# Optimization experiments

Hardware: AMD Instinct MI355X
Metric: run time of the kernel (lower is better)

Reference implementation:

```python
import jax, jax.numpy as jnp
import numpy as np


def setup_inputs() -> dict:
    key = jax.random.key(0)
    ks = jax.random.split(key, 6)
    B, S, DK = 4, 2048, 1024
    scale = 1.0 / np.sqrt(DK)  # keep weight magnitudes sane like torch init
    return {
        "q": jax.random.normal(ks[0], (B, S, DK), jnp.float32),
        "k": jax.random.normal(ks[1], (B, S, DK), jnp.float32),
        "v": jax.random.normal(ks[2], (B, S, DK), jnp.float32),
        "wq": jax.random.normal(ks[3], (DK, DK), jnp.float32) * scale,
        "wk": jax.random.normal(ks[4], (DK, DK), jnp.float32) * scale,
        "wv": jax.random.normal(ks[5], (DK, DK), jnp.float32) * scale,
    }


def reference(q, k, v, wq, wk, wv):
    dk = q.shape[-1]
    # nn.Linear: y = x @ W^T  (weights stored [out, in])
    qp = jnp.einsum("bsd,ed->bse", q, wq)
    kp = jnp.einsum("bsd,ed->bse", k, wk)
    vp = jnp.einsum("bsd,ed->bse", v, wv)
    norm = 1.0 / jnp.sqrt(jnp.asarray(dk, qp.dtype))
    s = jnp.einsum("bqd,bkd->bqk", qp, kp) * norm  # [B, S, S]
    # module computes exp(s)/sum(exp(s)) manually; mathematically softmax
    e = jnp.exp(s)
    attention = e / jnp.sum(e, axis=-1, keepdims=True)
    # dropout is identity in eval mode (deterministic reference)
    return jnp.einsum("bqk,bkd->bqd", attention, vp)
```

## Files before the change

kernel.cpp:

```cpp
#include <hip/hip_runtime.h>

typedef _Float16 f16;
typedef _Float16 f16x4 __attribute__((ext_vector_type(4)));
typedef _Float16 f16x8 __attribute__((ext_vector_type(8)));
typedef float    fx4   __attribute__((ext_vector_type(4)));

#define MODE_PROJ   0
#define MODE_SCORES 1
#define MODE_PV     2

constexpr int Bsz = 4;
constexpr int S   = 2048;
constexpr int DK  = 1024;
constexpr int BM = 128, BN = 128, BK = 64;
constexpr long SD   = (long)S * DK;
constexpr long SS   = (long)S * S;
constexpr long BIGN = (long)Bsz * S * DK;

__device__ __forceinline__ void glds16(const f16* g, f16* l) {
    __builtin_amdgcn_global_load_lds(
        (const __attribute__((address_space(1))) void*)g,
        (__attribute__((address_space(3))) void*)l, 16, 0, 0);
}

__global__ __launch_bounds__(256)
void convert_kernel(const float* q, const float* k, const float* v,
                    const float* wq, const float* wk, const float* wv)
{
    int bx = blockIdx.x;
    const float* src;
    int blk;
    if (bx < 12288) {
        int t = bx >> 12; blk = bx & 4095;
        src = (t == 0) ? q : (t == 1) ? k : v;
    } else {
        int u = bx - 12288;
        int t = u >> 9; blk = u & 511;
        src = (t == 0) ? wq : (t == 1) ? wk : wv;
    }
    size_t off = (size_t)blk * 2048 + (size_t)threadIdx.x * 8;
    float4 f0 = *(const float4*)(src + off);
    float4 f1 = *(const float4*)(src + off + 4);
    __syncthreads();
    f16x8 h = {(f16)f0.x, (f16)f0.y, (f16)f0.z, (f16)f0.w,
               (f16)f1.x, (f16)f1.y, (f16)f1.z, (f16)f1.w};
    *(f16x8*)((char*)src + (size_t)blk * 8192 + (size_t)threadIdx.x * 16) = h;
}

__device__ __forceinline__ size_t pp(int r, int c) {
    return ((size_t)(r >> 1) << 12) + ((r & 1) << 10) + c;
}

template<int MODE>
__global__ __launch_bounds__(256, 4)
void gemm_kernel(const f16* A0, const f16* A1, const f16* A2,
                 const f16* B0, const f16* B1, const f16* B2,
                 void* O0, void* O1, float* rowsum,
                 int lda, int ldb, int K, int ldo)
{
    __shared__ f16 lA[BM * BK];
    __shared__ f16 lB[BN * BK];

    const int tid = threadIdx.x;
    const int id  = blockIdx.x;
    const int z   = blockIdx.y;
    int row0, col0;
    if constexpr (MODE == MODE_PROJ) { row0 = (id & 63) * BM; col0 = (id >> 6) * BN; }
    else                             { row0 = (id & 15) * BM; col0 = (id >> 4) * BN; }

    const int lane = tid & 63;
    const int quad = lane >> 4;
    const int cn   = lane & 15;
    const int w    = tid >> 6;
    const int wm   = w >> 1;
    const int wn   = w & 1;

    const f16 *Ap, *Bp;
    if constexpr (MODE == MODE_PROJ) {
        Ap = (z == 0) ? A0 : (z == 1) ? A1 : A2;
        Bp = (z == 0) ? B0 : (z == 1) ? B1 : B2;
    } else if constexpr (MODE == MODE_SCORES) {
        Ap = A0 + (long)z * SD;  Bp = B0 + (long)z * SD;
        rowsum += (long)z * S;
    } else {
        Ap = A0 + (long)z * SS;  Bp = B0 + (long)z * SD;
        rowsum += (long)z * S;
    }

    fx4 acc[4][4];
    #pragma unroll
    for (int mt = 0; mt < 4; ++mt)
        #pragma unroll
        for (int nt = 0; nt < 4; ++nt)
            acc[mt][nt] = (fx4){0.f, 0.f, 0.f, 0.f};

    const int lr8 = lane >> 3;
    const int swc = (lane & 7) ^ lr8;
    const int lcS = swc << 3;

    for (int k0 = 0; k0 < K; k0 += BK) {
        __syncthreads();
        #pragma unroll
        for (int i = 0; i < 4; ++i) {
            int rb = w * 32 + i * 8;
            if constexpr (MODE == MODE_PROJ) {
                glds16(Ap + pp(row0 + rb + lr8, k0 + lcS), &lA[rb * BK]);
                glds16(Bp + pp(col0 + rb + lr8, k0 + lcS), &lB[rb * BK]);
            } else {
                glds16(Ap + (size_t)(row0 + rb + lr8) * lda + k0 + lcS, &lA[rb * BK]);
                glds16(Bp + (size_t)(col0 + rb + lr8) * ldb + k0 + lcS, &lB[rb * BK]);
            }
        }
        __syncthreads();

        #pragma unroll
        for (int kh = 0; kh < 2; ++kh) {
            f16x8 af[4], bf[4];
            #pragma unroll
            for (int mt = 0; mt < 4; ++mt) {
                int r = wm * 64 + mt * 16 + cn;
                int ch = ((kh << 2) | quad) ^ (r & 7);
                af[mt] = *(const f16x8*)&lA[r * BK + ch * 8];
            }
            #pragma unroll
            for (int nt = 0; nt < 4; ++nt) {
                int r = wn * 64 + nt * 16 + cn;
                int ch = ((kh << 2) | quad) ^ (r & 7);
                bf[nt] = *(const f16x8*)&lB[r * BK + ch * 8];
            }
            #pragma unroll
            for (int mt = 0; mt < 4; ++mt)
                #pragma unroll
                for (int nt = 0; nt < 4; ++nt)
                    acc[mt][nt] = __builtin_amdgcn_mfma_f32_16x16x32_f16(
                        af[mt], bf[nt], acc[mt][nt], 0, 0, 0);
        }
    }

    if constexpr (MODE == MODE_PROJ) {
        if (z < 2) {
            f16* O = (f16*)O0 + (long)z * BIGN;
            #pragma unroll
            for (int mt = 0; mt < 4; ++mt) {
                int r0 = row0 + wm * 64 + mt * 16 + quad * 4;
                #pragma unroll
                for (int nt = 0; nt < 4; ++nt) {
                    int c = col0 + wn * 64 + nt * 16 + cn;
                    #pragma unroll
                    for (int reg = 0; reg < 4; ++reg)
                        O[(size_t)(r0 + reg) * DK + c] = (f16)acc[mt][nt][reg];
                }
            }
        } else {
            #pragma unroll
            for (int mt = 0; mt < 4; ++mt) {
                int r0 = row0 + wm * 64 + mt * 16 + quad * 4;
                int b  = r0 >> 11;
                int s  = r0 & 2047;
                f16* O = (f16*)O1 + (long)b * SD;
                #pragma unroll
                for (int nt = 0; nt < 4; ++nt) {
                    int c = col0 + wn * 64 + nt * 16 + cn;
                    f16x4 h = {(f16)acc[mt][nt][0], (f16)acc[mt][nt][1],
                               (f16)acc[mt][nt][2], (f16)acc[mt][nt][3]};
                    *(f16x4*)&O[(size_t)c * S + s] = h;
                }
            }
        }
    } else if constexpr (MODE == MODE_SCORES) {
        f16* O = (f16*)O0 + (long)z * SS;
        const float sl2e = 0.03125f * 1.44269504f;
        float rs[4][4];
        #pragma unroll
        for (int mt = 0; mt < 4; ++mt)
            #pragma unroll
            for (int reg = 0; reg < 4; ++reg) rs[mt][reg] = 0.f;
        #pragma unroll
        for (int mt = 0; mt < 4; ++mt) {
            int r0 = row0 + wm * 64 + mt * 16 + quad * 4;
            #pragma unroll
            for (int nt = 0; nt < 4; ++nt) {
                int c = col0 + wn * 64 + nt * 16 + cn;
                #pragma unroll
                for (int reg = 0; reg < 4; ++reg) {
                    float vv = exp2f(acc[mt][nt][reg] * sl2e);
                    rs[mt][reg] += vv;
                    O[(size_t)(r0 + reg) * ldo + c] = (f16)vv;
                }
            }
        }
        #pragma unroll
        for (int mt = 0; mt < 4; ++mt) {
            int r0 = row0 + wm * 64 + mt * 16 + quad * 4;
            #pragma unroll
            for (int reg = 0; reg < 4; ++reg) {
                float vv = rs[mt][reg];
                vv += __shfl_xor(vv, 1);
                vv += __shfl_xor(vv, 2);
                vv += __shfl_xor(vv, 4);
                vv += __shfl_xor(vv, 8);
                if (cn == 0) atomicAdd(&rowsum[r0 + reg], vv);
            }
        }
    } else {
        float* O = (float*)O0 + (long)z * SD;
        #pragma unroll
        for (int mt = 0; mt < 4; ++mt) {
            int r0 = row0 + wm * 64 + mt * 16 + quad * 4;
            fx4 rsv = *(const fx4*)&rowsum[r0];
            fx4 inv = {1.f / rsv[0], 1.f / rsv[1], 1.f / rsv[2], 1.f / rsv[3]};
            #pragma unroll
            for (int nt = 0; nt < 4; ++nt) {
                int c = col0 + wn * 64 + nt * 16 + cn;
                #pragma unroll
                for (int reg = 0; reg < 4; ++reg)
                    O[(size_t)(r0 + reg) * ldo + c] = acc[mt][nt][reg] * inv[reg];
            }
        }
    }
}

extern "C" void kernel_launch(void* const* d_in, const int* in_sizes, int n_in,
                              void* d_out, int out_size, void* d_ws, size_t ws_size,
                              hipStream_t stream) {
    const float* q  = (const float*)d_in[0];
    const float* k  = (const float*)d_in[1];
    const float* v  = (const float*)d_in[2];
    const float* wq = (const float*)d_in[3];
    const float* wk = (const float*)d_in[4];
    const float* wv = (const float*)d_in[5];
    float* out = (float*)d_out;

    char* ws = (char*)d_ws;
    f16*   qp     = (f16*)(ws);
    f16*   kp     = (f16*)(ws + ((size_t)16 << 20));
    f16*   vpT    = (f16*)(ws + ((size_t)32 << 20));
    f16*   E      = (f16*)(ws + ((size_t)48 << 20));
    float* rowsum = (float*)(ws + ((size_t)80 << 20));

    hipMemsetAsync(rowsum, 0, (size_t)Bsz * S * sizeof(float), stream);

    convert_kernel<<<13824, 256, 0, stream>>>(q, k, v, wq, wk, wv);

    const f16* qh  = (const f16*)q;
    const f16* kh  = (const f16*)k;
    const f16* vh  = (const f16*)v;
    const f16* wqh = (const f16*)wq;
    const f16* wkh = (const f16*)wk;
    const f16* wvh = (const f16*)wv;

    dim3 blk(256);
    gemm_kernel<MODE_PROJ><<<dim3(512, 3), blk, 0, stream>>>(
        qh, kh, vh, wqh, wkh, wvh, qp, vpT, nullptr, DK, DK, DK, DK);
    gemm_kernel<MODE_SCORES><<<dim3(256, 4), blk, 0, stream>>>(
        qp, nullptr, nullptr, kp, nullptr, nullptr, E, nullptr, rowsum,
        DK, DK, DK, S);
    gemm_kernel<MODE_PV><<<dim3(128, 4), blk, 0, stream>>>(
        E, nullptr, nullptr, vpT, nullptr, nullptr, out, nullptr, rowsum,
        S, S, S, DK);
}
```

Measured before the change: 296.2 us.

## Double-buffer LDS and widen GEMM tile to 128x256 with 8 waves

```diff
diff --git a/kernel.cpp b/kernel.cpp
--- a/kernel.cpp
+++ b/kernel.cpp
@@ -12,7 +12,7 @@
 constexpr int Bsz = 4;
 constexpr int S   = 2048;
 constexpr int DK  = 1024;
-constexpr int BM = 128, BN = 128, BK = 64;
+constexpr int BM = 128, BN = 256, BK = 64;
 constexpr long SD   = (long)S * DK;
 constexpr long SS   = (long)S * S;
 constexpr long BIGN = (long)Bsz * S * DK;
@@ -52,14 +52,14 @@
 }
 
 template<int MODE>
-__global__ __launch_bounds__(256, 4)
+__global__ __launch_bounds__(512, 2)
 void gemm_kernel(const f16* A0, const f16* A1, const f16* A2,
                  const f16* B0, const f16* B1, const f16* B2,
                  void* O0, void* O1, float* rowsum,
                  int lda, int ldb, int K, int ldo)
 {
-    __shared__ f16 lA[BM * BK];
-    __shared__ f16 lB[BN * BK];
+    __shared__ __attribute__((aligned(16))) f16 lA[2][BM * BK];
+    __shared__ __attribute__((aligned(16))) f16 lB[2][BN * BK];
 
     const int tid = threadIdx.x;
     const int id  = blockIdx.x;
@@ -72,8 +72,8 @@
     const int quad = lane >> 4;
     const int cn   = lane & 15;
     const int w    = tid >> 6;
-    const int wm   = w >> 1;
-    const int wn   = w & 1;
+    const int wm   = w >> 2;
+    const int wn   = w & 3;
 
     const f16 *Ap, *Bp;
     if constexpr (MODE == MODE_PROJ) {
@@ -98,44 +98,98 @@
     const int swc = (lane & 7) ^ lr8;
     const int lcS = swc << 3;
 
-    for (int k0 = 0; k0 < K; k0 += BK) {
+    f16x8 af[4];
+    f16x8 bf[8];
+
+#define STAGE(BUF, K0) do {                                                          \
+    _Pragma("unroll")                                                                \
+    for (int i_ = 0; i_ < 2; ++i_) {                                                 \
+        int rb_ = w * 16 + i_ * 8;                                                   \
+        if constexpr (MODE == MODE_PROJ)                                             \
+            glds16(Ap + pp(row0 + rb_ + lr8, (K0) + lcS), &lA[BUF][rb_ * BK]);       \
+        else                                                                         \
+            glds16(Ap + (size_t)(row0 + rb_ + lr8) * lda + (K0) + lcS,               \
+                   &lA[BUF][rb_ * BK]);                                              \
+    }                                                                                \
+    _Pragma("unroll")                                                                \
+    for (int i_ = 0; i_ < 4; ++i_) {                                                 \
+        int rb_ = w * 32 + i_ * 8;                                                   \
+        if constexpr (MODE == MODE_PROJ)                                             \
+            glds16(Bp + pp(col0 + rb_ + lr8, (K0) + lcS), &lB[BUF][rb_ * BK]);       \
+        else                                                                         \
+            glds16(Bp + (size_t)(col0 + rb_ + lr8) * ldb + (K0) + lcS,               \
+                   &lB[BUF][rb_ * BK]);                                              \
+    }                                                                                \
+} while (0)
+
+#define LDA_FRAGS(BUF, MH) do {                                                      \
+    _Pragma("unroll")                                                                \
+    for (int m_ = 0; m_ < 2; ++m_)                                                   \
+        _Pragma("unroll")                                                            \
+        for (int kk_ = 0; kk_ < 2; ++kk_) {                                          \
+            int r_  = wm * 64 + ((MH) * 2 + m_) * 16 + cn;                           \
+            int ch_ = ((kk_ << 2) | quad) ^ (r_ & 7);                                \
+            af[m_ * 2 + kk_] = *(const f16x8*)&lA[BUF][r_ * BK + ch_ * 8];           \
+        }                                                                            \
+} while (0)
+
+#define LDB_FRAGS(BUF, NH) do {                                                      \
+    _Pragma("unroll")                                                                \
+    for (int n_ = 0; n_ < 2; ++n_)                                                   \
+        _Pragma("unroll")                                                            \
+        for (int kk_ = 0; kk_ < 2; ++kk_) {                                          \
+            int nt_ = (NH) * 2 + n_;                                                 \
+            int r_  = wn * 64 + nt_ * 16 + cn;                                       \
+            int ch_ = ((kk_ << 2) | quad) ^ (r_ & 7);                                \
+            bf[nt_ * 2 + kk_] = *(const f16x8*)&lB[BUF][r_ * BK + ch_ * 8];          \
+        }                                                                            \
+} while (0)
+
+#define QUAD_MFMA(MH, NH) do {                                                       \
+    __builtin_amdgcn_s_setprio(1);                                                   \
+    _Pragma("unroll")                                                                \
+    for (int m_ = 0; m_ < 2; ++m_)                                                   \
+        _Pragma("unroll")                                                            \
+        for (int n_ = 0; n_ < 2; ++n_) {                                             \
+            _Pragma("unroll")                                                        \
+            for (int kk_ = 0; kk_ < 2; ++kk_)                                        \
+                acc[(MH) * 2 + m_][(NH) * 2 + n_] =                                  \
+                    __builtin_amdgcn_mfma_f32_16x16x32_f16(                          \
+                        af[m_ * 2 + kk_], bf[((NH) * 2 + n_) * 2 + kk_],             \
+                        acc[(MH) * 2 + m_][(NH) * 2 + n_], 0, 0, 0);                 \
+        }                                                                            \
+    __builtin_amdgcn_s_setprio(0);                                                   \
+} while (0)
+
+    const int ntile = K / BK;
+    STAGE(0, 0);
+    __syncthreads();
+    int bufc = 0;
+    for (int t = 0; t < ntile; ++t) {
+        const int k0 = t * BK;
+        LDA_FRAGS(bufc, 0);
+        LDB_FRAGS(bufc, 0);
+        if (t + 1 < ntile) STAGE(bufc ^ 1, k0 + BK);
+        __builtin_amdgcn_s_barrier();
+        QUAD_MFMA(0, 0);
+        __builtin_amdgcn_s_barrier();
+        LDB_FRAGS(bufc, 1);
+        __builtin_amdgcn_s_barrier();
+        QUAD_MFMA(0, 1);
+        __builtin_amdgcn_s_barrier();
+        LDA_FRAGS(bufc, 1);
+        __builtin_amdgcn_s_barrier();
+        QUAD_MFMA(1, 1);
+        __builtin_amdgcn_s_barrier();
+        QUAD_MFMA(1, 0);
         __syncthreads();
-        #pragma unroll
-        for (int i = 0; i < 4; ++i) {
-            int rb = w * 32 + i * 8;
-            if constexpr (MODE == MODE_PROJ) {
-                glds16(Ap + pp(row0 + rb + lr8, k0 + lcS), &lA[rb * BK]);
-                glds16(Bp + pp(col0 + rb + lr8, k0 + lcS), &lB[rb * BK]);
-            } else {
-                glds16(Ap + (size_t)(row0 + rb + lr8) * lda + k0 + lcS, &lA[rb * BK]);
-                glds16(Bp + (size_t)(col0 + rb + lr8) * ldb + k0 + lcS, &lB[rb * BK]);
-            }
-        }
-        __syncthreads();
-
-        #pragma unroll
-        for (int kh = 0; kh < 2; ++kh) {
-            f16x8 af[4], bf[4];
-            #pragma unroll
-            for (int mt = 0; mt < 4; ++mt) {
-                int r = wm * 64 + mt * 16 + cn;
-                int ch = ((kh << 2) | quad) ^ (r & 7);
-                af[mt] = *(const f16x8*)&lA[r * BK + ch * 8];
-            }
-            #pragma unroll
-            for (int nt = 0; nt < 4; ++nt) {
-                int r = wn * 64 + nt * 16 + cn;
-                int ch = ((kh << 2) | quad) ^ (r & 7);
-                bf[nt] = *(const f16x8*)&lB[r * BK + ch * 8];
-            }
-            #pragma unroll
-            for (int mt = 0; mt < 4; ++mt)
-                #pragma unroll
-                for (int nt = 0; nt < 4; ++nt)
-                    acc[mt][nt] = __builtin_amdgcn_mfma_f32_16x16x32_f16(
-                        af[mt], bf[nt], acc[mt][nt], 0, 0, 0);
-        }
+        bufc ^= 1;
     }
+
+#undef STAGE
+#undef LDA_FRAGS
+#undef LDB_FRAGS
+#undef QUAD_MFMA
 
     if constexpr (MODE == MODE_PROJ) {
         if (z < 2) {
@@ -249,13 +303,13 @@
     const f16* wkh = (const f16*)wk;
     const f16* wvh = (const f16*)wv;
 
-    dim3 blk(256);
-    gemm_kernel<MODE_PROJ><<<dim3(512, 3), blk, 0, stream>>>(
+    dim3 blk(512);
+    gemm_kernel<MODE_PROJ><<<dim3(256, 3), blk, 0, stream>>>(
         qh, kh, vh, wqh, wkh, wvh, qp, vpT, nullptr, DK, DK, DK, DK);
-    gemm_kernel<MODE_SCORES><<<dim3(256, 4), blk, 0, stream>>>(
+    gemm_kernel<MODE_SCORES><<<dim3(128, 4), blk, 0, stream>>>(
         qp, nullptr, nullptr, kp, nullptr, nullptr, E, nullptr, rowsum,
         DK, DK, DK, S);
-    gemm_kernel<MODE_PV><<<dim3(128, 4), blk, 0, stream>>>(
+    gemm_kernel<MODE_PV><<<dim3(64, 4), blk, 0, stream>>>(
         E, nullptr, nullptr, vpT, nullptr, nullptr, out, nullptr, rowsum,
         S, S, S, DK);
 }
```

Measured after the change: 309.0 us. 1.04x slower.

## Add 256x256-tile 8-wave pipelined GEMM for projection and score stages

Applied to the files above, without the earlier changes.

```diff
diff --git a/kernel.cpp b/kernel.cpp
--- a/kernel.cpp
+++ b/kernel.cpp
@@ -51,6 +51,265 @@
     return ((size_t)(r >> 1) << 12) + ((r & 1) << 10) + c;
 }
 
+
+#define VW6 asm volatile("s_waitcnt vmcnt(6)" ::: "memory")
+#define VW4 asm volatile("s_waitcnt vmcnt(4)" ::: "memory")
+#define VW2 asm volatile("s_waitcnt vmcnt(2)" ::: "memory")
+#define VW0 asm volatile("s_waitcnt vmcnt(0)" ::: "memory")
+#define VWX do {} while (0)
+
+template<int MODE>
+__global__ __launch_bounds__(512, 2)
+void gemm8p_kernel(const f16* A0_, const f16* A1_, const f16* A2_,
+                   const f16* B0_, const f16* B1_, const f16* B2_,
+                   void* O0, void* O1, float* rowsum,
+                   int lda, int ldb, int K, int ldo)
+{
+    __shared__ __attribute__((aligned(16))) f16 lA[2][2][128 * 64];
+    __shared__ __attribute__((aligned(16))) f16 lB[2][2][128 * 64];
+
+    const int tid = threadIdx.x;
+    const int id  = blockIdx.x;
+    const int z   = blockIdx.y;
+    int row0, col0;
+    if constexpr (MODE == MODE_PROJ) { row0 = (id & 31) * 256; col0 = (id >> 5) * 256; }
+    else                             { row0 = (id & 7)  * 256; col0 = (id >> 3) * 256; }
+
+    const int lane = tid & 63;
+    const int quad = lane >> 4;
+    const int cn   = lane & 15;
+    const int w    = tid >> 6;
+    const int wm   = w >> 2;
+    const int wn   = w & 3;
+
+    const f16 *Ap, *Bp;
+    if constexpr (MODE == MODE_PROJ) {
+        Ap = (z == 0) ? A0_ : (z == 1) ? A1_ : A2_;
+        Bp = (z == 0) ? B0_ : (z == 1) ? B1_ : B2_;
+    } else {
+        Ap = A0_ + (long)z * SD;  Bp = B0_ + (long)z * SD;
+        rowsum += (long)z * S;
+    }
+
+    fx4 acc[8][4];
+    #pragma unroll
+    for (int am = 0; am < 8; ++am)
+        #pragma unroll
+        for (int an = 0; an < 4; ++an)
+            acc[am][an] = (fx4){0.f, 0.f, 0.f, 0.f};
+
+    const int lr8 = lane >> 3;
+    const int swc = (lane & 7) ^ lr8;
+    const int lcS = swc << 3;
+
+    f16x8 af[8];
+    f16x8 bf0[4];
+    f16x8 bf1[4];
+
+#define STAGE_A0(BUF, K0) do {                                               \
+    _Pragma("unroll")                                                        \
+    for (int i_ = 0; i_ < 2; ++i_) {                                         \
+        int Lb_ = w * 16 + i_ * 8;                                           \
+        int rb_ = ((Lb_ >> 6) << 7) | (Lb_ & 63);                            \
+        f16* d_ = &lA[BUF][rb_ >> 7][(rb_ & 127) * 64];                      \
+        int gr_ = row0 + rb_ + lr8;                                          \
+        if constexpr (MODE == MODE_PROJ)                                     \
+            glds16(Ap + pp(gr_, (K0) + lcS), d_);                            \
+        else                                                                 \
+            glds16(Ap + (size_t)gr_ * lda + (K0) + lcS, d_);                 \
+    }                                                                        \
+} while (0)
+
+#define STAGE_A1(BUF, K0) do {                                               \
+    _Pragma("unroll")                                                        \
+    for (int i_ = 0; i_ < 2; ++i_) {                                         \
+        int Lb_ = w * 16 + i_ * 8;                                           \
+        int rb_ = (((Lb_ >> 6) << 7) | (Lb_ & 63)) + 64;                     \
+        f16* d_ = &lA[BUF][rb_ >> 7][(rb_ & 127) * 64];                      \
+        int gr_ = row0 + rb_ + lr8;                                          \
+        if constexpr (MODE == MODE_PROJ)                                     \
+            glds16(Ap + pp(gr_, (K0) + lcS), d_);                            \
+        else                                                                 \
+            glds16(Ap + (size_t)gr_ * lda + (K0) + lcS, d_);                 \
+    }                                                                        \
+} while (0)
+
+#define STAGE_B0(BUF, K0) do {                                               \
+    _Pragma("unroll")                                                        \
+    for (int i_ = 0; i_ < 2; ++i_) {                                         \
+        int Lb_ = w * 16 + i_ * 8;                                           \
+        int rb_ = ((Lb_ >> 5) << 6) | (Lb_ & 31);                            \
+        f16* d_ = &lB[BUF][rb_ >> 7][(rb_ & 127) * 64];                      \
+        int gr_ = col0 + rb_ + lr8;                                          \
+        if constexpr (MODE == MODE_PROJ)                                     \
+            glds16(Bp + pp(gr_, (K0) + lcS), d_);                            \
+        else                                                                 \
+            glds16(Bp + (size_t)gr_ * ldb + (K0) + lcS, d_);                 \
+    }                                                                        \
+} while (0)
+
+#define STAGE_B1(BUF, K0) do {                                               \
+    _Pragma("unroll")                                                        \
+    for (int i_ = 0; i_ < 2; ++i_) {                                         \
+        int Lb_ = w * 16 + i_ * 8;                                           \
+        int rb_ = (((Lb_ >> 5) << 6) | (Lb_ & 31)) + 32;                     \
+        f16* d_ = &lB[BUF][rb_ >> 7][(rb_ & 127) * 64];                      \
+        int gr_ = col0 + rb_ + lr8;                                          \
+        if constexpr (MODE == MODE_PROJ)                                     \
+            glds16(Bp + pp(gr_, (K0) + lcS), d_);                            \
+        else                                                                 \
+            glds16(Bp + (size_t)gr_ * ldb + (K0) + lcS, d_);                 \
+    }                                                                        \
+} while (0)
+
+#define LDA(BUF, MH) do {                                                    \
+    _Pragma("unroll")                                                        \
+    for (int mf_ = 0; mf_ < 4; ++mf_)                                        \
+        _Pragma("unroll")                                                    \
+        for (int kk_ = 0; kk_ < 2; ++kk_) {                                  \
+            int rr_ = (MH) * 64 + mf_ * 16 + cn;                             \
+            int ch_ = ((kk_ << 2) | quad) ^ (cn & 7);                        \
+            af[mf_ * 2 + kk_] = *(const f16x8*)&lA[BUF][wm][rr_ * 64 + ch_ * 8]; \
+        }                                                                    \
+} while (0)
+
+#define LDB(BUF, NH, BFA) do {                                               \
+    _Pragma("unroll")                                                        \
+    for (int nf_ = 0; nf_ < 2; ++nf_)                                        \
+        _Pragma("unroll")                                                    \
+        for (int kk_ = 0; kk_ < 2; ++kk_) {                                  \
+            int rr_ = (wn & 1) * 64 + (NH) * 32 + nf_ * 16 + cn;             \
+            int ch_ = ((kk_ << 2) | quad) ^ (cn & 7);                        \
+            BFA[nf_ * 2 + kk_] = *(const f16x8*)&lB[BUF][wn >> 1][rr_ * 64 + ch_ * 8]; \
+        }                                                                    \
+} while (0)
+
+#define PH_MFMA(MH, NH, BFA) do {                                            \
+    __builtin_amdgcn_s_setprio(1);                                           \
+    _Pragma("unroll")                                                        \
+    for (int mf_ = 0; mf_ < 4; ++mf_)                                        \
+        _Pragma("unroll")                                                    \
+        for (int nf_ = 0; nf_ < 2; ++nf_)                                    \
+            _Pragma("unroll")                                                \
+            for (int kk_ = 0; kk_ < 2; ++kk_)                                \
+                acc[(MH) * 4 + mf_][(NH) * 2 + nf_] =                        \
+                    __builtin_amdgcn_mfma_f32_16x16x32_f16(                  \
+                        af[mf_ * 2 + kk_], BFA[nf_ * 2 + kk_],               \
+                        acc[(MH) * 4 + mf_][(NH) * 2 + nf_], 0, 0, 0);       \
+    __builtin_amdgcn_s_setprio(0);                                           \
+} while (0)
+
+#define TILE(K0, BUF, STG, A0N, W0S, W1S, W2S, W3S) do {                     \
+                                                    \
+    LDA(BUF, 0);                                                             \
+    LDB(BUF, 0, bf0);                                                        \
+    if (STG) STAGE_B0((BUF) ^ 1, (K0) + BK);                                 \
+    __builtin_amdgcn_s_barrier();                                            \
+    PH_MFMA(0, 0, bf0);                                                      \
+    W0S; __builtin_amdgcn_s_barrier();                                       \
+                                                    \
+    LDB(BUF, 1, bf1);                                                        \
+    if (STG) STAGE_B1((BUF) ^ 1, (K0) + BK);                                 \
+    __builtin_amdgcn_s_barrier();                                            \
+    PH_MFMA(0, 1, bf1);                                                      \
+    W1S; __builtin_amdgcn_s_barrier();                                       \
+                                                    \
+    LDA(BUF, 1);                                                             \
+    if (STG) STAGE_A1((BUF) ^ 1, (K0) + BK);                                 \
+    __builtin_amdgcn_s_barrier();                                            \
+    PH_MFMA(1, 1, bf1);                                                      \
+    W2S; __builtin_amdgcn_s_barrier();                                       \
+      \
+    if (A0N) STAGE_A0((BUF), (K0) + 2 * BK);                                 \
+    PH_MFMA(1, 0, bf0);                                                      \
+    W3S; __builtin_amdgcn_s_barrier();                                       \
+} while (0)
+
+    const int ntile = K / BK;
+    STAGE_A0(0, 0); STAGE_B0(0, 0); STAGE_B1(0, 0); STAGE_A1(0, 0);
+    STAGE_A0(1, BK);
+    VW6; __builtin_amdgcn_s_barrier();
+
+    for (int t = 0; t < ntile - 2; t += 2) {
+        TILE(t * BK,       0, 1, 1, VW6, VW6, VW6, VW6);
+        TILE((t + 1) * BK, 1, 1, 1, VW6, VW6, VW6, VW6);
+    }
+    TILE((ntile - 2) * BK, 0, 1, 0, VW6, VW6, VW6, VW4);
+    TILE((ntile - 1) * BK, 1, 0, 0, VW2, VW0, VWX, VWX);
+
+#undef STAGE_A0
+#undef STAGE_A1
+#undef STAGE_B0
+#undef STAGE_B1
+#undef LDA
+#undef LDB
+#undef PH_MFMA
+#undef TILE
+
+    if constexpr (MODE == MODE_PROJ) {
+        if (z < 2) {
+            f16* O = (f16*)O0 + (long)z * BIGN;
+            #pragma unroll
+            for (int am = 0; am < 8; ++am) {
+                int r0 = row0 + wm * 128 + am * 16 + quad * 4;
+                #pragma unroll
+                for (int an = 0; an < 4; ++an) {
+                    int c = col0 + wn * 64 + an * 16 + cn;
+                    #pragma unroll
+                    for (int reg = 0; reg < 4; ++reg)
+                        O[(size_t)(r0 + reg) * DK + c] = (f16)acc[am][an][reg];
+                }
+            }
+        } else {
+            #pragma unroll
+            for (int am = 0; am < 8; ++am) {
+                int r0 = row0 + wm * 128 + am * 16 + quad * 4;
+                int b  = r0 >> 11;
+                int s  = r0 & 2047;
+                f16* O = (f16*)O1 + (long)b * SD;
+                #pragma unroll
+                for (int an = 0; an < 4; ++an) {
+                    int c = col0 + wn * 64 + an * 16 + cn;
+                    f16x4 h = {(f16)acc[am][an][0], (f16)acc[am][an][1],
+                               (f16)acc[am][an][2], (f16)acc[am][an][3]};
+                    *(f16x4*)&O[(size_t)c * S + s] = h;
+                }
+            }
+        }
+    } else {
+        f16* O = (f16*)O0 + (long)z * SS;
+        const float sl2e = 0.03125f * 1.44269504f;
+        #pragma unroll
+        for (int am = 0; am < 8; ++am) {
+            int r0 = row0 + wm * 128 + am * 16 + quad * 4;
+            #pragma unroll
+            for (int an = 0; an < 4; ++an) {
+                int c = col0 + wn * 64 + an * 16 + cn;
+                #pragma unroll
+                for (int reg = 0; reg < 4; ++reg) {
+                    float vv = exp2f(acc[am][an][reg] * sl2e);
+                    acc[am][an][reg] = vv;
+                    O[(size_t)(r0 + reg) * ldo + c] = (f16)vv;
+                }
+            }
+        }
+        #pragma unroll
+        for (int am = 0; am < 8; ++am) {
+            int r0 = row0 + wm * 128 + am * 16 + quad * 4;
+            #pragma unroll
+            for (int reg = 0; reg < 4; ++reg) {
+                float vv = acc[am][0][reg] + acc[am][1][reg] +
+                           acc[am][2][reg] + acc[am][3][reg];
+                vv += __shfl_xor(vv, 1);
+                vv += __shfl_xor(vv, 2);
+                vv += __shfl_xor(vv, 4);
+                vv += __shfl_xor(vv, 8);
+                if (cn == 0) atomicAdd(&rowsum[r0 + reg], vv);
+            }
+        }
+    }
+}
+
 template<int MODE>
 __global__ __launch_bounds__(256, 4)
 void gemm_kernel(const f16* A0, const f16* A1, const f16* A2,
@@ -249,13 +508,12 @@
     const f16* wkh = (const f16*)wk;
     const f16* wvh = (const f16*)wv;
 
-    dim3 blk(256);
-    gemm_kernel<MODE_PROJ><<<dim3(512, 3), blk, 0, stream>>>(
+    gemm8p_kernel<MODE_PROJ><<<dim3(128, 3), 512, 0, stream>>>(
         qh, kh, vh, wqh, wkh, wvh, qp, vpT, nullptr, DK, DK, DK, DK);
-    gemm_kernel<MODE_SCORES><<<dim3(256, 4), blk, 0, stream>>>(
+    gemm8p_kernel<MODE_SCORES><<<dim3(64, 4), 512, 0, stream>>>(
         qp, nullptr, nullptr, kp, nullptr, nullptr, E, nullptr, rowsum,
         DK, DK, DK, S);
-    gemm_kernel<MODE_PV><<<dim3(128, 4), blk, 0, stream>>>(
+    gemm_kernel<MODE_PV><<<dim3(128, 4), 256, 0, stream>>>(
         E, nullptr, nullptr, vpT, nullptr, nullptr, out, nullptr, rowsum,
         S, S, S, DK);
 }
```

After: 303.9 us. 1.03x slower.
